# Kernel optimization log

Hardware: AMD Instinct MI355X
Metric: run time of the kernel (lower is better)

The kernel has to match this reference:

```python
import jax, jax.numpy as jnp
import numpy as np

N, B, E, H = 16384, 16, 131072, 2
NPG = N // B  # nodes per graph
DIMS = [128, 256, 512]  # in==out channels per GAT layer


def setup_inputs() -> dict:
    key = jax.random.key(0)
    ks = iter(jax.random.split(key, 40))
    inp = {"node_feats": jax.random.normal(next(ks), (N, DIMS[0]), jnp.float32)}
    for l, d in enumerate(DIMS):
        s = 1.0 / np.sqrt(d)
        inp[f"W{l}"] = jax.random.normal(next(ks), (d, H * d), jnp.float32) * s
        inp[f"attnl{l}"] = jax.random.normal(next(ks), (H, d), jnp.float32) * 0.1
        inp[f"attnr{l}"] = jax.random.normal(next(ks), (H, d), jnp.float32) * 0.1
        inp[f"resW{l}"] = jax.random.normal(next(ks), (d, H * d), jnp.float32) * s
        inp[f"gamma{l}"] = jnp.ones((d,), jnp.float32)
        inp[f"beta{l}"] = jnp.zeros((d,), jnp.float32)
        inp[f"alpha{l}"] = jnp.ones((d,), jnp.float32)
    dst = jax.random.randint(next(ks), (E,), 0, N, jnp.int32)
    # source node sampled from the same graph as the destination
    src = (dst // NPG) * NPG + jax.random.randint(next(ks), (E,), 0, NPG, jnp.int32)
    inp["edge_src"] = src
    inp["edge_dst"] = dst
    inp["graph_ids"] = jnp.repeat(jnp.arange(B, dtype=jnp.int32), NPG)
    return inp


def _gat(x, W, al, ar, rW, src, dst, d):
    # x: [N, in]; W,rW: [in, H*d]; al,ar: [H,d]
    h = (x @ W).reshape(N, H, d)
    el = jnp.sum(h * al, -1)  # [N,H]
    er = jnp.sum(h * ar, -1)  # [N,H]
    e = jax.nn.leaky_relu(el[src] + er[dst], 0.2)  # [E,H]
    m = jax.ops.segment_max(e, dst, num_segments=N)
    ex = jnp.exp(e - m[dst])
    a = ex / jax.ops.segment_sum(ex, dst, num_segments=N)[dst]  # edge softmax
    out = jax.ops.segment_sum(h[src] * a[:, :, None], dst, num_segments=N)
    return out + (x @ rW).reshape(N, H, d)  # residual projection


def _gnorm(x, gamma, beta, alpha, eps=1e-5):
    # GraphNorm: (x - alpha*mean) / std * gamma + beta, stats over all nodes/heads
    mean = jnp.mean(x, axis=(0, 1), keepdims=True)
    sh = x - alpha * mean
    var = jnp.mean(sh * sh, axis=(0, 1), keepdims=True)
    return gamma * sh * jax.lax.rsqrt(var + eps) + beta


def reference(node_feats, W0, attnl0, attnr0, resW0, gamma0, beta0, alpha0,
              W1, attnl1, attnr1, resW1, gamma1, beta1, alpha1,
              W2, attnl2, attnr2, resW2, gamma2, beta2, alpha2,
              edge_src, edge_dst, graph_ids):
    params = [(W0, attnl0, attnr0, resW0, gamma0, beta0, alpha0),
              (W1, attnl1, attnr1, resW1, gamma1, beta1, alpha1),
              (W2, attnl2, attnr2, resW2, gamma2, beta2, alpha2)]
    counts = jax.ops.segment_sum(jnp.ones((N,), jnp.float32), graph_ids, num_segments=B)
    x = node_feats
    parts = []
    for l, d in enumerate(DIMS):
        W, al, ar, rW, g, b, a_ = params[l]
        x = _gat(x.reshape(N, -1), W, al, ar, rW, edge_src, edge_dst, d)  # [N,H,d]
        x = _gnorm(x, g, b, a_)
        x = jax.nn.leaky_relu(x, 0.01)
        nm = x.mean(1)  # [N,d] head-mean stored as 'updated_feats'
        parts.append(jax.ops.segment_sum(nm, graph_ids, num_segments=B) / counts[:, None])
    return jax.nn.leaky_relu(jnp.concatenate(parts, -1), 0.01)  # [B, 896]
```

## Files before the change

### kernel.cpp

```cpp
#include <hip/hip_runtime.h>
#include <math.h>

constexpr int NNODES  = 16384;
constexpr int NEDGES  = 131072;
constexpr int NGRAPHS = 16;

typedef short bf16x8 __attribute__((ext_vector_type(8)));
typedef short bf16x4 __attribute__((ext_vector_type(4)));
typedef float f32x4  __attribute__((ext_vector_type(4)));

__device__ __forceinline__ float leaky(float x, float s){ return x >= 0.0f ? x : s * x; }

__device__ __forceinline__ unsigned short f2bf(float f){
  unsigned u = __builtin_bit_cast(unsigned, f);
  u += 0x7FFFu + ((u >> 16) & 1u);
  return (unsigned short)(u >> 16);
}
__device__ __forceinline__ float bf2f(unsigned short u){
  unsigned x = (unsigned)u << 16; return __builtin_bit_cast(float, x);
}

__device__ __forceinline__ void gload_lds16(const unsigned short* g, unsigned short* l){
  __builtin_amdgcn_global_load_lds((const __attribute__((address_space(1))) void*)g,
                                   (__attribute__((address_space(3))) void*)l, 16, 0, 0);
}

__global__ void k_deg(const int* __restrict__ dst, int* __restrict__ deg){
  int e = blockIdx.x * 256 + threadIdx.x;
  if (e < NEDGES) atomicAdd(&deg[dst[e]], 1);
}

__global__ __launch_bounds__(1024) void k_scan(const int* __restrict__ deg,
                                               int* __restrict__ rowptr,
                                               int* __restrict__ cursor){
  __shared__ int sums[1024];
  int t = threadIdx.x;
  int loc[16];
  int s = 0;
  #pragma unroll
  for (int i = 0; i < 16; i++){ loc[i] = deg[t*16 + i]; s += loc[i]; }
  sums[t] = s; __syncthreads();
  for (int off = 1; off < 1024; off <<= 1){
    int v = (t >= off) ? sums[t - off] : 0;
    __syncthreads();
    sums[t] += v;
    __syncthreads();
  }
  int base = (t > 0) ? sums[t-1] : 0;
  #pragma unroll
  for (int i = 0; i < 16; i++){
    rowptr[t*16 + i] = base; cursor[t*16 + i] = base; base += loc[i];
  }
  if (t == 1023) rowptr[NNODES] = base;
}

__global__ void k_scatter(const int* __restrict__ src, const int* __restrict__ dst,
                          int* __restrict__ cursor, int* __restrict__ perm){
  int e = blockIdx.x * 256 + threadIdx.x;
  if (e < NEDGES){ int p = atomicAdd(&cursor[dst[e]], 1); perm[p] = src[e]; }
}

__global__ __launch_bounds__(256) void k_counts(const int* __restrict__ gid, float* __restrict__ counts){
  __shared__ int h[NGRAPHS];
  int t = threadIdx.x;
  if (t < NGRAPHS) h[t] = 0;
  __syncthreads();
  int base = blockIdx.x * 1024;
  #pragma unroll
  for (int i = 0; i < 4; i++)
    atomicAdd(&h[gid[base + t + i*256]], 1);
  __syncthreads();
  if (t < NGRAPHS && h[t] > 0) atomicAdd(&counts[t], (float)h[t]);
}

__global__ void k_cvt(const float* __restrict__ in, unsigned short* __restrict__ out, int n4){
  int i = blockIdx.x * 256 + threadIdx.x;
  if (i >= n4) return;
  float4 v = ((const float4*)in)[i];
  ushort4 o; o.x = f2bf(v.x); o.y = f2bf(v.y); o.z = f2bf(v.z); o.w = f2bf(v.w);
  ((ushort4*)out)[i] = o;
}

__global__ __launch_bounds__(256) void k_cvt_t(const float* __restrict__ W,
                                               unsigned short* __restrict__ Wt,
                                               int K, int NN){
  __shared__ float tile[32][33];
  int n0 = blockIdx.x * 32, k0 = blockIdx.y * 32;
  int tx = threadIdx.x & 31, ty = threadIdx.x >> 5;
  #pragma unroll
  for (int i = 0; i < 4; i++)
    tile[ty + i*8][tx] = W[(size_t)(k0 + ty + i*8) * NN + n0 + tx];
  __syncthreads();
  #pragma unroll
  for (int i = 0; i < 4; i++)
    Wt[(size_t)(n0 + ty + i*8) * K + k0 + tx] = f2bf(tile[tx][ty + i*8]);
}

__global__ __launch_bounds__(256) void k_gemm2(const unsigned short* __restrict__ A,
                                               const unsigned short* __restrict__ Wt,
                                               const unsigned short* __restrict__ RWt,
                                               unsigned short* __restrict__ HB,
                                               unsigned short* __restrict__ RB,
                                               int K, int NN){
  __shared__ unsigned short As[2][128 * 64];
  __shared__ unsigned short Bs[2][128 * 64];
  int t = threadIdx.x;
  int lane = t & 63, w = t >> 6;
  int nx  = gridDim.x;
  int nwg = nx * gridDim.y;
  int bid = blockIdx.x + blockIdx.y * nx;
  int wg  = (bid & 7) * (nwg >> 3) + (bid >> 3);
  int bx = wg % nx, by = wg / nx;
  int half = nx >> 1;
  bool isW = bx < half;
  const unsigned short* Bt = isW ? Wt : RWt;
  int colB = (isW ? bx : bx - half) * 128;
  int rowA = by * 128;

  int wr = (w >> 1) * 64, wc = (w & 1) * 64;
  int l16 = lane & 15, lhi = lane >> 4;
  int r8  = lane >> 3;
  int kcs = (((lane & 7) * 16) ^ (r8 << 4)) >> 1;
  f32x4 acc[4][4] = {};

  const unsigned short* Ap = A  + (size_t)(rowA) * K + kcs;
  const unsigned short* Bp = Bt + (size_t)(colB) * K + kcs;

  int nt = K >> 6;
  #pragma unroll
  for (int i = 0; i < 4; i++){
    int c = w * 4 + i;
    int row = c * 8 + r8;
    gload_lds16(Ap + (size_t)row * K, &As[0][c * 512]);
    gload_lds16(Bp + (size_t)row * K, &Bs[0][c * 512]);
  }
  __syncthreads();

  int cur = 0;
  for (int tI = 0; tI < nt; tI++){
    if (tI + 1 < nt){
      int k0n = (tI + 1) << 6;
      #pragma unroll
      for (int i = 0; i < 4; i++){
        int c = w * 4 + i;
        int row = c * 8 + r8;
        gload_lds16(Ap + (size_t)row * K + k0n, &As[cur ^ 1][c * 512]);
        gload_lds16(Bp + (size_t)row * K + k0n, &Bs[cur ^ 1][c * 512]);
      }
    }
    bf16x8 af[4][2], bfr[4][2];
    #pragma unroll
    for (int mi = 0; mi < 4; mi++){
      int row = wr + mi * 16 + l16;
      #pragma unroll
      for (int s = 0; s < 2; s++){
        int k = s * 32 + lhi * 8;
        int off = row * 128 + ((k * 2) ^ ((row & 7) << 4));
        af[mi][s] = *(const bf16x8*)((const char*)As[cur] + off);
      }
    }
    #pragma unroll
    for (int ni = 0; ni < 4; ni++){
      int row = wc + ni * 16 + l16;
      #pragma unroll
      for (int s = 0; s < 2; s++){
        int k = s * 32 + lhi * 8;
        int off = row * 128 + ((k * 2) ^ ((row & 7) << 4));
        bfr[ni][s] = *(const bf16x8*)((const char*)Bs[cur] + off);
      }
    }
    #pragma unroll
    for (int mi = 0; mi < 4; mi++)
      #pragma unroll
      for (int ni = 0; ni < 4; ni++){
        acc[mi][ni] = __builtin_amdgcn_mfma_f32_16x16x32_bf16(af[mi][0], bfr[ni][0], acc[mi][ni], 0, 0, 0);
        acc[mi][ni] = __builtin_amdgcn_mfma_f32_16x16x32_bf16(af[mi][1], bfr[ni][1], acc[mi][ni], 0, 0, 0);
      }
    __syncthreads();
    cur ^= 1;
  }

  unsigned short* C = isW ? HB : RB;
  #pragma unroll
  for (int mi = 0; mi < 4; mi++){
    #pragma unroll
    for (int j = 0; j < 4; j++){
      int r = rowA + wr + mi * 16 + lhi * 4 + j;
      unsigned short* Cp = C + (size_t)r * NN + colB + wc + l16;
      #pragma unroll
      for (int ni = 0; ni < 4; ni++)
        Cp[ni * 16] = f2bf(acc[mi][ni][j]);
    }
  }
}

template<int D>
__global__ __launch_bounds__(256) void k_elr(const unsigned short* __restrict__ HB,
                                             const float* __restrict__ al,
                                             const float* __restrict__ ar,
                                             float* __restrict__ el, float* __restrict__ er){
  constexpr int ITER = (2*D)/256;
  int wid = threadIdx.x >> 6, lane = threadIdx.x & 63;
  int n = blockIdx.x * 4 + wid;
  const unsigned short* hrow = HB + (size_t)n * (2*D);
  float sl[2] = {0.f, 0.f}, sr[2] = {0.f, 0.f};
  #pragma unroll
  for (int j = 0; j < ITER; j++){
    int base = j*256 + lane*4;
    bf16x4 v = *(const bf16x4*)(hrow + base);
    int hh = (base < D) ? 0 : 1;
    #pragma unroll
    for (int i = 0; i < 4; i++){
      float f = bf2f((unsigned short)v[i]);
      sl[hh] += f * al[base + i];
      sr[hh] += f * ar[base + i];
    }
  }
  #pragma unroll
  for (int o = 32; o; o >>= 1){
    sl[0] += __shfl_xor(sl[0], o); sl[1] += __shfl_xor(sl[1], o);
    sr[0] += __shfl_xor(sr[0], o); sr[1] += __shfl_xor(sr[1], o);
  }
  if (lane < 2){ el[n*2 + lane] = sl[lane]; er[n*2 + lane] = sr[lane]; }
}

template<int D>
__global__ __launch_bounds__(256) void k_attn(const unsigned short* __restrict__ HB,
                                              unsigned short* __restrict__ RB,
                                              const float* __restrict__ el,
                                              const float* __restrict__ er,
                                              const int* __restrict__ rowptr,
                                              const int* __restrict__ perm){
  constexpr int ITER = (2*D)/256;
  int wid = threadIdx.x >> 6, lane = threadIdx.x & 63;
  int nb = (blockIdx.x & 7) * (NNODES/4/8) + (blockIdx.x >> 3);
  int n = nb * 4 + wid;
  int r0 = rowptr[n], r1 = rowptr[n+1];
  if (r0 == r1) return;
  float er0 = er[n*2], er1 = er[n*2+1];
  float mx0 = -1e30f, mx1 = -1e30f;
  for (int e = r0 + lane; e < r1; e += 64){
    int s = perm[e];
    mx0 = fmaxf(mx0, leaky(el[s*2]   + er0, 0.2f));
    mx1 = fmaxf(mx1, leaky(el[s*2+1] + er1, 0.2f));
  }
  #pragma unroll
  for (int o = 32; o; o >>= 1){ mx0 = fmaxf(mx0, __shfl_xor(mx0, o)); mx1 = fmaxf(mx1, __shfl_xor(mx1, o)); }
  float sm0 = 0.0f, sm1 = 0.0f;
  for (int e = r0 + lane; e < r1; e += 64){
    int s = perm[e];
    sm0 += expf(leaky(el[s*2]   + er0, 0.2f) - mx0);
    sm1 += expf(leaky(el[s*2+1] + er1, 0.2f) - mx1);
  }
  #pragma unroll
  for (int o = 32; o; o >>= 1){ sm0 += __shfl_xor(sm0, o); sm1 += __shfl_xor(sm1, o); }
  float inv0 = 1.0f / sm0, inv1 = 1.0f / sm1;
  float acc[ITER][4];
  #pragma unroll
  for (int j = 0; j < ITER; j++)
    #pragma unroll
    for (int i = 0; i < 4; i++) acc[j][i] = 0.0f;
  for (int e = r0; e < r1; ++e){
    int s = perm[e];
    float a0 = expf(leaky(el[s*2]   + er0, 0.2f) - mx0) * inv0;
    float a1 = expf(leaky(el[s*2+1] + er1, 0.2f) - mx1) * inv1;
    const unsigned short* hrow = HB + (size_t)s * (2*D);
    #pragma unroll
    for (int j = 0; j < ITER; j++){
      int base = j*256 + lane*4;
      bf16x4 v = *(const bf16x4*)(hrow + base);
      float a = (base < D) ? a0 : a1;
      #pragma unroll
      for (int i = 0; i < 4; i++)
        acc[j][i] += a * bf2f((unsigned short)v[i]);
    }
  }
  unsigned short* rrow = RB + (size_t)n * (2*D);
  #pragma unroll
  for (int j = 0; j < ITER; j++){
    int base = j*256 + lane*4;
    bf16x4 r = *(bf16x4*)(rrow + base);
    ushort4 o;
    o.x = f2bf(bf2f((unsigned short)r[0]) + acc[j][0]);
    o.y = f2bf(bf2f((unsigned short)r[1]) + acc[j][1]);
    o.z = f2bf(bf2f((unsigned short)r[2]) + acc[j][2]);
    o.w = f2bf(bf2f((unsigned short)r[3]) + acc[j][3]);
    *(ushort4*)(rrow + base) = o;
  }
}

__global__ __launch_bounds__(256) void k_stats(const unsigned short* __restrict__ R, int nn,
                                               float* __restrict__ gsum, float* __restrict__ gsq){
  int t = threadIdx.x, lane = t & 63, w = t >> 6;
  int c = blockIdx.y * 256 + lane * 4;
  const unsigned short* base = R + (size_t)(blockIdx.x * 128 + w) * nn + c;
  float4 s = make_float4(0,0,0,0), q = make_float4(0,0,0,0);
  #pragma unroll 4
  for (int i = 0; i < 32; i++){
    bf16x4 bv = *(const bf16x4*)(base + (size_t)(i * 4) * nn);
    float vx = bf2f((unsigned short)bv[0]), vy = bf2f((unsigned short)bv[1]);
    float vz = bf2f((unsigned short)bv[2]), vw = bf2f((unsigned short)bv[3]);
    s.x += vx; s.y += vy; s.z += vz; s.w += vw;
    q.x += vx*vx; q.y += vy*vy; q.z += vz*vz; q.w += vw*vw;
  }
  __shared__ float4 rs[256], rq[256];
  rs[t] = s; rq[t] = q; __syncthreads();
  if (t < 64){
    float4 a = rs[t], b = rs[t+64], c2 = rs[t+128], d2 = rs[t+192];
    float4 e = rq[t], f = rq[t+64], g2 = rq[t+128], h2 = rq[t+192];
    int cc = blockIdx.y * 256 + t * 4;
    atomicAdd(&gsum[cc+0], a.x+b.x+c2.x+d2.x);
    atomicAdd(&gsum[cc+1], a.y+b.y+c2.y+d2.y);
    atomicAdd(&gsum[cc+2], a.z+b.z+c2.z+d2.z);
    atomicAdd(&gsum[cc+3], a.w+b.w+c2.w+d2.w);
    atomicAdd(&gsq [cc+0], e.x+f.x+g2.x+h2.x);
    atomicAdd(&gsq [cc+1], e.y+f.y+g2.y+h2.y);
    atomicAdd(&gsq [cc+2], e.z+f.z+g2.z+h2.z);
    atomicAdd(&gsq [cc+3], e.w+f.w+g2.w+h2.w);
  }
}

__global__ void k_finstats(const float* __restrict__ gsum, const float* __restrict__ gsq,
                           const float* __restrict__ alpha,
                           float* __restrict__ mean, float* __restrict__ rstd, int d){
  int t = threadIdx.x;
  if (t >= d) return;
  float s = gsum[t] + gsum[t + d];
  float q = gsq[t]  + gsq[t + d];
  const float M = (float)(2 * NNODES);
  float m   = s / M;
  float msq = q / M;
  float a   = alpha[t];
  float var = msq - a * m * m * (2.0f - a);
  mean[t] = m;
  rstd[t] = rsqrtf(var + 1e-5f);
}

__global__ __launch_bounds__(256) void k_norm_pool(const unsigned short* __restrict__ R,
                                                   unsigned short* __restrict__ Xn,
                                                   const float* __restrict__ mean,
                                                   const float* __restrict__ rstd,
                                                   const float* __restrict__ gamma,
                                                   const float* __restrict__ beta,
                                                   const float* __restrict__ alpha,
                                                   float* __restrict__ pool, int d, int loff){
  int t = threadIdx.x, lane = t & 63, w = t >> 6;
  int c = blockIdx.y * 256 + lane * 4;
  int cm = c & (d - 1);
  int nodeb = blockIdx.x * 128;
  int g = blockIdx.x >> 3;
  int nn = 2 * d;
  float4 mm = *(const float4*)(mean + cm);
  float4 rr = *(const float4*)(rstd + cm);
  float4 gg = *(const float4*)(gamma + cm);
  float4 bb = *(const float4*)(beta + cm);
  float4 aa = *(const float4*)(alpha + cm);
  float am0 = aa.x*mm.x, am1 = aa.y*mm.y, am2 = aa.z*mm.z, am3 = aa.w*mm.w;
  const unsigned short* base = R + (size_t)(nodeb + w) * nn + c;
  unsigned short* xb = Xn ? (Xn + (size_t)(nodeb + w) * nn + c) : nullptr;
  float4 accp = make_float4(0,0,0,0);
  #pragma unroll 4
  for (int i = 0; i < 32; i++){
    bf16x4 bv = *(const bf16x4*)(base + (size_t)(i * 4) * nn);
    float vx = bf2f((unsigned short)bv[0]), vy = bf2f((unsigned short)bv[1]);
    float vz = bf2f((unsigned short)bv[2]), vw = bf2f((unsigned short)bv[3]);
    float y0 = gg.x*(vx-am0)*rr.x + bb.x; y0 = y0 >= 0.f ? y0 : 0.01f*y0;
    float y1 = gg.y*(vy-am1)*rr.y + bb.y; y1 = y1 >= 0.f ? y1 : 0.01f*y1;
    float y2 = gg.z*(vz-am2)*rr.z + bb.z; y2 = y2 >= 0.f ? y2 : 0.01f*y2;
    float y3 = gg.w*(vw-am3)*rr.w + bb.w; y3 = y3 >= 0.f ? y3 : 0.01f*y3;
    if (xb){
      ushort4 o; o.x = f2bf(y0); o.y = f2bf(y1); o.z = f2bf(y2); o.w = f2bf(y3);
      *(ushort4*)(xb + (size_t)(i * 4) * nn) = o;
    }
    accp.x += y0; accp.y += y1; accp.z += y2; accp.w += y3;
  }
  __shared__ float4 red[256];
  red[t] = accp; __syncthreads();
  if (t < 64){
    float4 a = red[t], b = red[t+64], c2 = red[t+128], d2 = red[t+192];
    int cc = blockIdx.y * 256 + t * 4;
    float* pb = pool + g * 896 + loff;
    atomicAdd(&pb[(cc+0) & (d-1)], 0.5f*(a.x+b.x+c2.x+d2.x));
    atomicAdd(&pb[(cc+1) & (d-1)], 0.5f*(a.y+b.y+c2.y+d2.y));
    atomicAdd(&pb[(cc+2) & (d-1)], 0.5f*(a.z+b.z+c2.z+d2.z));
    atomicAdd(&pb[(cc+3) & (d-1)], 0.5f*(a.w+b.w+c2.w+d2.w));
  }
}

__global__ void k_final(const float* __restrict__ pool, const float* __restrict__ counts,
                        float* __restrict__ out){
  int idx = blockIdx.x * 256 + threadIdx.x;
  if (idx >= NGRAPHS * 896) return;
  int g = idx / 896;
  float v = pool[idx] / counts[g];
  out[idx] = v >= 0.0f ? v : 0.01f * v;
}

extern "C" void kernel_launch(void* const* d_in, const int* in_sizes, int n_in,
                              void* d_out, int out_size, void* d_ws, size_t ws_size,
                              hipStream_t stream){
  const float* x0 = (const float*)d_in[0];
  const float *W[3], *AL[3], *AR[3], *RW[3], *GA[3], *BE[3], *ALP[3];
  for (int l = 0; l < 3; l++){
    const int b = 1 + l*7;
    W[l]  = (const float*)d_in[b+0];
    AL[l] = (const float*)d_in[b+1];
    AR[l] = (const float*)d_in[b+2];
    RW[l] = (const float*)d_in[b+3];
    GA[l] = (const float*)d_in[b+4];
    BE[l] = (const float*)d_in[b+5];
    ALP[l]= (const float*)d_in[b+6];
  }
  const int* esrc = (const int*)d_in[22];
  const int* edst = (const int*)d_in[23];
  const int* gid  = (const int*)d_in[24];
  float* out = (float*)d_out;

  char* p = (char*)d_ws;
  auto carve = [&](size_t bytes)->void*{
    void* r = (void*)p; p += (bytes + 255) & ~(size_t)255; return r;
  };
  unsigned short* HB = (unsigned short*)carve((size_t)NNODES * 1024 * 2);
  unsigned short* RB = (unsigned short*)carve((size_t)NNODES * 1024 * 2);
  unsigned short* X0b = (unsigned short*)carve((size_t)NNODES * 128 * 2);
  unsigned short* XA  = (unsigned short*)carve((size_t)NNODES * 256 * 2);
  unsigned short* XB  = (unsigned short*)carve((size_t)NNODES * 512 * 2);
  unsigned short* Wt  = (unsigned short*)carve((size_t)1024 * 512 * 2);
  unsigned short* RWt = (unsigned short*)carve((size_t)1024 * 512 * 2);
  float* el     = (float*)carve((size_t)NNODES * 2 * 4);
  float* er     = (float*)carve((size_t)NNODES * 2 * 4);
  int*   deg    = (int*)  carve((size_t)NNODES * 4);
  int*   rowptr = (int*)  carve((size_t)(NNODES + 1) * 4);
  int*   cursor = (int*)  carve((size_t)NNODES * 4);
  int*   perm   = (int*)  carve((size_t)NEDGES * 4);
  float* stats  = (float*)carve(2048 * 4);
  float* meanb  = (float*)carve(512 * 4);
  float* rstdb  = (float*)carve(512 * 4);
  float* pool   = (float*)carve((size_t)NGRAPHS * 896 * 4);
  float* countsF= (float*)carve((size_t)NGRAPHS * 4);
  (void)ws_size; (void)in_sizes; (void)n_in; (void)out_size;

  hipMemsetAsync(deg, 0, NNODES * 4, stream);
  hipMemsetAsync(pool, 0, NGRAPHS * 896 * 4, stream);
  hipMemsetAsync(countsF, 0, NGRAPHS * 4, stream);

  k_deg    <<<NEDGES/256, 256, 0, stream>>>(edst, deg);
  k_scan   <<<1, 1024, 0, stream>>>(deg, rowptr, cursor);
  k_scatter<<<NEDGES/256, 256, 0, stream>>>(esrc, edst, cursor, perm);
  k_counts <<<NNODES/1024, 256, 0, stream>>>(gid, countsF);
  k_cvt    <<<(NNODES*128/4 + 255)/256, 256, 0, stream>>>(x0, X0b, NNODES*128/4);

  const unsigned short* xin = X0b;
  int loff = 0;
  const int dims[3] = {128, 256, 512};
  for (int l = 0; l < 3; l++){
    int d = dims[l], nn = 2*d;
    dim3 gt(nn/32, d/32);
    k_cvt_t<<<gt, 256, 0, stream>>>(W[l],  Wt,  d, nn);
    k_cvt_t<<<gt, 256, 0, stream>>>(RW[l], RWt, d, nn);
    dim3 gg(2*nn/128, NNODES/128);
    k_gemm2<<<gg, 256, 0, stream>>>(xin, Wt, RWt, HB, RB, d, nn);
    if (d == 128){
      k_elr <128><<<NNODES/4, 256, 0, stream>>>(HB, AL[l], AR[l], el, er);
      k_attn<128><<<NNODES/4, 256, 0, stream>>>(HB, RB, el, er, rowptr, perm);
    } else if (d == 256){
      k_elr <256><<<NNODES/4, 256, 0, stream>>>(HB, AL[l], AR[l], el, er);
      k_attn<256><<<NNODES/4, 256, 0, stream>>>(HB, RB, el, er, rowptr, perm);
    } else {
      k_elr <512><<<NNODES/4, 256, 0, stream>>>(HB, AL[l], AR[l], el, er);
      k_attn<512><<<NNODES/4, 256, 0, stream>>>(HB, RB, el, er, rowptr, perm);
    }
    hipMemsetAsync(stats, 0, 2048 * 4, stream);
    dim3 gs(NNODES/128, nn/256);
    k_stats   <<<gs, 256, 0, stream>>>(RB, nn, stats, stats + 1024);
    k_finstats<<<1, 512, 0, stream>>>(stats, stats + 1024, ALP[l], meanb, rstdb, d);
    unsigned short* xn = (l == 0) ? XA : (l == 1) ? XB : nullptr;
    k_norm_pool<<<gs, 256, 0, stream>>>(RB, xn, meanb, rstdb, GA[l], BE[l], ALP[l], pool, d, loff);
    xin = xn; loff += d;
  }
  k_final<<<(NGRAPHS*896 + 255)/256, 256, 0, stream>>>(pool, countsF, out);
}
```

Baseline: 351.0 us.

## Share A tile across W and residual projections in GEMM, merge weight conversions

The GEMM kernel now computes both the attention projection and the residual projection in one block. Each loaded A tile is reused for two accumulator sets, which halves the grid and the number of A loads. Double buffering is removed in favour of a single-stage load/sync loop, and accumulator register pressure doubles, which may lower occupancy and drop load/compute overlap. The two weight transpose-convert launches are also merged into one launch using blockIdx.z.

```diff
diff --git a/kernel.cpp b/kernel.cpp
--- a/kernel.cpp
+++ b/kernel.cpp
@@ -81,19 +81,23 @@
   ((ushort4*)out)[i] = o;
 }
 
-__global__ __launch_bounds__(256) void k_cvt_t(const float* __restrict__ W,
-                                               unsigned short* __restrict__ Wt,
-                                               int K, int NN){
+__global__ __launch_bounds__(256) void k_cvt_t2(const float* __restrict__ W,
+                                                const float* __restrict__ RW,
+                                                unsigned short* __restrict__ Wt,
+                                                unsigned short* __restrict__ RWt,
+                                                int K, int NN){
   __shared__ float tile[32][33];
+  const float* src = blockIdx.z ? RW : W;
+  unsigned short* dst = blockIdx.z ? RWt : Wt;
   int n0 = blockIdx.x * 32, k0 = blockIdx.y * 32;
   int tx = threadIdx.x & 31, ty = threadIdx.x >> 5;
   #pragma unroll
   for (int i = 0; i < 4; i++)
-    tile[ty + i*8][tx] = W[(size_t)(k0 + ty + i*8) * NN + n0 + tx];
+    tile[ty + i*8][tx] = src[(size_t)(k0 + ty + i*8) * NN + n0 + tx];
   __syncthreads();
   #pragma unroll
   for (int i = 0; i < 4; i++)
-    Wt[(size_t)(n0 + ty + i*8) * K + k0 + tx] = f2bf(tile[tx][ty + i*8]);
+    dst[(size_t)(n0 + ty + i*8) * K + k0 + tx] = f2bf(tile[tx][ty + i*8]);
 }
 
 __global__ __launch_bounds__(256) void k_gemm2(const unsigned short* __restrict__ A,
@@ -102,8 +106,9 @@
                                                unsigned short* __restrict__ HB,
                                                unsigned short* __restrict__ RB,
                                                int K, int NN){
-  __shared__ unsigned short As[2][128 * 64];
-  __shared__ unsigned short Bs[2][128 * 64];
+  __shared__ unsigned short As[128 * 64];
+  __shared__ unsigned short Ws[128 * 64];
+  __shared__ unsigned short Rs[128 * 64];
   int t = threadIdx.x;
   int lane = t & 63, w = t >> 6;
   int nx  = gridDim.x;
@@ -111,85 +116,71 @@
   int bid = blockIdx.x + blockIdx.y * nx;
   int wg  = (bid & 7) * (nwg >> 3) + (bid >> 3);
   int bx = wg % nx, by = wg / nx;
-  int half = nx >> 1;
-  bool isW = bx < half;
-  const unsigned short* Bt = isW ? Wt : RWt;
-  int colB = (isW ? bx : bx - half) * 128;
+  int colB = bx * 128;
   int rowA = by * 128;
 
   int wr = (w >> 1) * 64, wc = (w & 1) * 64;
   int l16 = lane & 15, lhi = lane >> 4;
   int r8  = lane >> 3;
   int kcs = (((lane & 7) * 16) ^ (r8 << 4)) >> 1;
-  f32x4 acc[4][4] = {};
-
-  const unsigned short* Ap = A  + (size_t)(rowA) * K + kcs;
-  const unsigned short* Bp = Bt + (size_t)(colB) * K + kcs;
-
-  int nt = K >> 6;
-  #pragma unroll
-  for (int i = 0; i < 4; i++){
-    int c = w * 4 + i;
-    int row = c * 8 + r8;
-    gload_lds16(Ap + (size_t)row * K, &As[0][c * 512]);
-    gload_lds16(Bp + (size_t)row * K, &Bs[0][c * 512]);
-  }
-  __syncthreads();
-
-  int cur = 0;
-  for (int tI = 0; tI < nt; tI++){
-    if (tI + 1 < nt){
-      int k0n = (tI + 1) << 6;
+
+  f32x4 accW[4][4] = {};
+  f32x4 accR[4][4] = {};
+
+  const unsigned short* Ap = A   + (size_t)rowA * K + kcs;
+  const unsigned short* Wp = Wt  + (size_t)colB * K + kcs;
+  const unsigned short* Rp = RWt + (size_t)colB * K + kcs;
+
+  for (int k0 = 0; k0 < K; k0 += 64){
+    __syncthreads();
+    #pragma unroll
+    for (int i = 0; i < 4; i++){
+      int c = w * 4 + i;
+      size_t go = (size_t)(c * 8 + r8) * K + k0;
+      gload_lds16(Ap + go, &As[c * 512]);
+      gload_lds16(Wp + go, &Ws[c * 512]);
+      gload_lds16(Rp + go, &Rs[c * 512]);
+    }
+    __syncthreads();
+    #pragma unroll
+    for (int s = 0; s < 2; s++){
+      int k = s * 32 + lhi * 8;
+      bf16x8 af[4], bw[4], br[4];
       #pragma unroll
-      for (int i = 0; i < 4; i++){
-        int c = w * 4 + i;
-        int row = c * 8 + r8;
-        gload_lds16(Ap + (size_t)row * K + k0n, &As[cur ^ 1][c * 512]);
-        gload_lds16(Bp + (size_t)row * K + k0n, &Bs[cur ^ 1][c * 512]);
+      for (int mi = 0; mi < 4; mi++){
+        int row = wr + mi * 16 + l16;
+        int off = row * 128 + ((k * 2) ^ ((row & 7) << 4));
+        af[mi] = *(const bf16x8*)((const char*)As + off);
       }
-    }
-    bf16x8 af[4][2], bfr[4][2];
-    #pragma unroll
-    for (int mi = 0; mi < 4; mi++){
-      int row = wr + mi * 16 + l16;
-      #pragma unroll
-      for (int s = 0; s < 2; s++){
-        int k = s * 32 + lhi * 8;
-        int off = row * 128 + ((k * 2) ^ ((row & 7) << 4));
-        af[mi][s] = *(const bf16x8*)((const char*)As[cur] + off);
-      }
-    }
-    #pragma unroll
-    for (int ni = 0; ni < 4; ni++){
-      int row = wc + ni * 16 + l16;
-      #pragma unroll
-      for (int s = 0; s < 2; s++){
-        int k = s * 32 + lhi * 8;
-        int off = row * 128 + ((k * 2) ^ ((row & 7) << 4));
-        bfr[ni][s] = *(const bf16x8*)((const char*)Bs[cur] + off);
-      }
-    }
-    #pragma unroll
-    for (int mi = 0; mi < 4; mi++)
       #pragma unroll
       for (int ni = 0; ni < 4; ni++){
-        acc[mi][ni] = __builtin_amdgcn_mfma_f32_16x16x32_bf16(af[mi][0], bfr[ni][0], acc[mi][ni], 0, 0, 0);
-        acc[mi][ni] = __builtin_amdgcn_mfma_f32_16x16x32_bf16(af[mi][1], bfr[ni][1], acc[mi][ni], 0, 0, 0);
+        int row = wc + ni * 16 + l16;
+        int off = row * 128 + ((k * 2) ^ ((row & 7) << 4));
+        bw[ni] = *(const bf16x8*)((const char*)Ws + off);
+        br[ni] = *(const bf16x8*)((const char*)Rs + off);
       }
-    __syncthreads();
-    cur ^= 1;
-  }
-
-  unsigned short* C = isW ? HB : RB;
+      #pragma unroll
+      for (int mi = 0; mi < 4; mi++)
+        #pragma unroll
+        for (int ni = 0; ni < 4; ni++){
+          accW[mi][ni] = __builtin_amdgcn_mfma_f32_16x16x32_bf16(af[mi], bw[ni], accW[mi][ni], 0, 0, 0);
+          accR[mi][ni] = __builtin_amdgcn_mfma_f32_16x16x32_bf16(af[mi], br[ni], accR[mi][ni], 0, 0, 0);
+        }
+    }
+  }
+
   #pragma unroll
   for (int mi = 0; mi < 4; mi++){
     #pragma unroll
     for (int j = 0; j < 4; j++){
       int r = rowA + wr + mi * 16 + lhi * 4 + j;
-      unsigned short* Cp = C + (size_t)r * NN + colB + wc + l16;
+      unsigned short* Hp = HB + (size_t)r * NN + colB + wc + l16;
+      unsigned short* Rp2 = RB + (size_t)r * NN + colB + wc + l16;
       #pragma unroll
-      for (int ni = 0; ni < 4; ni++)
-        Cp[ni * 16] = f2bf(acc[mi][ni][j]);
+      for (int ni = 0; ni < 4; ni++){
+        Hp[ni * 16]  = f2bf(accW[mi][ni][j]);
+        Rp2[ni * 16] = f2bf(accR[mi][ni][j]);
+      }
     }
   }
 }
@@ -455,10 +446,9 @@
   const int dims[3] = {128, 256, 512};
   for (int l = 0; l < 3; l++){
     int d = dims[l], nn = 2*d;
-    dim3 gt(nn/32, d/32);
-    k_cvt_t<<<gt, 256, 0, stream>>>(W[l],  Wt,  d, nn);
-    k_cvt_t<<<gt, 256, 0, stream>>>(RW[l], RWt, d, nn);
-    dim3 gg(2*nn/128, NNODES/128);
+    dim3 gt(nn/32, d/32, 2);
+    k_cvt_t2<<<gt, 256, 0, stream>>>(W[l], RW[l], Wt, RWt, d, nn);
+    dim3 gg(nn/128, NNODES/128);
     k_gemm2<<<gg, 256, 0, stream>>>(xin, Wt, RWt, HB, RB, d, nn);
     if (d == 128){
       k_elr <128><<<NNODES/4, 256, 0, stream>>>(HB, AL[l], AR[l], el, er);
```

Result: slower. 368.5 us (+5.0%).
